# Kernel optimization log

Hardware: AMD Instinct MI355X
Metric: run time of the kernel (lower is better)

The kernel has to match this reference:

```python
import jax, jax.numpy as jnp
import numpy as np

N_HEAD = 16
ROPE_BASE = 10000.0


def _rotate_every_two(x):
    # x: [..., d]; pairs (x0,x1) -> (-x1, x0) interleaved (GPT-J style)
    x1 = x[..., ::2]
    x2 = x[..., 1::2]
    return jnp.stack((-x2, x1), axis=-1).reshape(x.shape)


def _rope_cos_sin(T, head_dim, dtype):
    inv_freq = 1.0 / (ROPE_BASE ** (jnp.arange(0, head_dim, 2, dtype=jnp.float32) / head_dim))
    t = jnp.arange(T, dtype=jnp.float32)
    freqs = t[:, None] * inv_freq[None, :]            # [T, hd/2]
    emb = jnp.repeat(freqs, 2, axis=-1)               # [T, hd], each freq duplicated
    return jnp.cos(emb).astype(dtype)[None, None], jnp.sin(emb).astype(dtype)[None, None]


def setup_inputs() -> dict:
    key = jax.random.key(0)
    k1, k2, k3 = jax.random.split(key, 3)
    C = 2048
    x = jax.random.normal(k1, (2, 2048, C), dtype=jnp.float32)
    Wqkv = jax.random.normal(k2, (C, 3 * C), dtype=jnp.float32) * 0.02   # c_attn.weight^T
    Wproj = jax.random.normal(k3, (C, C), dtype=jnp.float32) * 0.02      # c_proj.weight^T
    return {"x": x, "Wqkv": Wqkv, "Wproj": Wproj, "causal": 1}


def reference(x, Wqkv, Wproj, causal):
    B, T, C = x.shape
    H = N_HEAD
    hd = C // H

    qkv = x @ Wqkv                                    # [B,T,3C]
    q, k, v = jnp.split(qkv, 3, axis=-1)
    # -> [B,H,T,hd]
    q = q.reshape(B, T, H, hd).transpose(0, 2, 1, 3)
    k = k.reshape(B, T, H, hd).transpose(0, 2, 1, 3)
    v = v.reshape(B, T, H, hd).transpose(0, 2, 1, 3)

    cos, sin = _rope_cos_sin(T, hd, x.dtype)          # [1,1,T,hd]
    q = q * cos + _rotate_every_two(q) * sin
    k = k * cos + _rotate_every_two(k) * sin

    scale = 1.0 / jnp.sqrt(jnp.asarray(hd, dtype=x.dtype))
    scores = jnp.einsum('bhqd,bhkd->bhqk', q, k) * scale  # [B,H,T,T]
    if causal:
        mask = jnp.tril(jnp.ones((T, T), dtype=bool))
        scores = jnp.where(mask[None, None], scores, jnp.asarray(-1e30, dtype=scores.dtype))
    attn = jax.nn.softmax(scores, axis=-1)
    y = jnp.einsum('bhqk,bhkd->bhqd', attn, v)        # [B,H,T,hd]
    y = y.transpose(0, 2, 1, 3).reshape(B, T, C)
    return y @ Wproj
```

## Files before the change

### kernel.cpp

```cpp
#include <hip/hip_runtime.h>
#include <cmath>

typedef __bf16 bf16_t;
typedef __bf16 bf16x8 __attribute__((ext_vector_type(8)));
typedef __bf16 bf16x4 __attribute__((ext_vector_type(4)));
typedef float f32x4 __attribute__((ext_vector_type(4)));

#define T_SEQ 2048
#define C_DIM 2048
#define H_NUM 16
#define HD    128
#define KK    2048

__global__ void rope_table_kernel(float* __restrict__ ct, float* __restrict__ st) {
  int idx = blockIdx.x * 256 + threadIdx.x;
  int t = idx >> 6, i = idx & 63;
  double invf = pow(10000.0, -(double)i / 64.0);
  float ang = (float)t * (float)invf;
  ct[idx] = cosf(ang);
  st[idx] = sinf(ang);
}

__global__ void convert_bf16_kernel(const float* __restrict__ in, bf16_t* __restrict__ out, int n4) {
  int i = blockIdx.x * 256 + threadIdx.x;
  if (i >= n4) return;
  const float4 v = reinterpret_cast<const float4*>(in)[i];
  bf16x4 o;
  o[0] = (bf16_t)v.x; o[1] = (bf16_t)v.y; o[2] = (bf16_t)v.z; o[3] = (bf16_t)v.w;
  reinterpret_cast<bf16x4*>(out)[i] = o;
}

__global__ void transpose_convert_kernel(const float* __restrict__ in, bf16_t* __restrict__ out,
                                         int R, int Cc) {
  __shared__ __align__(16) bf16_t tile[32][33];
  int c0 = blockIdx.x * 32, r0 = blockIdx.y * 32;
  int tx = threadIdx.x, ty = threadIdx.y;
#pragma unroll
  for (int i = 0; i < 4; ++i)
    tile[ty + 8 * i][tx] = (bf16_t)in[(size_t)(r0 + ty + 8 * i) * Cc + c0 + tx];
  __syncthreads();
#pragma unroll
  for (int i = 0; i < 4; ++i)
    out[(size_t)(c0 + ty + 8 * i) * R + r0 + tx] = tile[tx][ty + 8 * i];
}

template <int MODE>
__global__ __launch_bounds__(256, 2)
void gemm_bf16_kernel(const bf16_t* __restrict__ A, const bf16_t* __restrict__ Bt,
                      float* __restrict__ outF,
                      bf16_t* __restrict__ qws, bf16_t* __restrict__ kws,
                      bf16_t* __restrict__ vtws,
                      const float* __restrict__ ctab, const float* __restrict__ stab) {
  const int tid = threadIdx.x;
  const int l = tid & 63, w = tid >> 6;
  const int wr = w >> 1, wc = w & 1;
  const int lg = l >> 4, lr = l & 15;

  const int g = blockIdx.x & 7;
  const int q = blockIdx.x >> 3;
  int m0, n0;
  if (MODE == 0) {
    m0 = (q / 6) * 128;
    n0 = (g * 6 + (q % 6)) * 128;
  } else {
    m0 = (g * 4 + (q & 3)) * 128;
    n0 = (q >> 2) * 128;
  }

  __shared__ __align__(16) bf16_t la[128][64];
  __shared__ __align__(16) bf16_t lb[128][64];

  f32x4 acc[4][4] = {};
  bf16x8 ra[4], rb[4];

  const bf16_t* Ab = A + (size_t)m0 * KK;
  const bf16_t* Bb = Bt + (size_t)n0 * KK;

#pragma unroll
  for (int c = 0; c < 4; ++c) {
    int p = tid + c * 256, row = p >> 3, kc = p & 7;
    ra[c] = *reinterpret_cast<const bf16x8*>(Ab + (size_t)row * KK + kc * 8);
    rb[c] = *reinterpret_cast<const bf16x8*>(Bb + (size_t)row * KK + kc * 8);
  }

  for (int kt = 0; kt < KK / 64; ++kt) {
    __syncthreads();
#pragma unroll
    for (int c = 0; c < 4; ++c) {
      int p = tid + c * 256, row = p >> 3;
      int kcw = (p & 7) ^ (row & 7);
      *reinterpret_cast<bf16x8*>(&la[row][kcw * 8]) = ra[c];
      *reinterpret_cast<bf16x8*>(&lb[row][kcw * 8]) = rb[c];
    }
    __syncthreads();
    if (kt + 1 < KK / 64) {
#pragma unroll
      for (int c = 0; c < 4; ++c) {
        int p = tid + c * 256, row = p >> 3, kc = p & 7;
        ra[c] = *reinterpret_cast<const bf16x8*>(Ab + (size_t)row * KK + (kt + 1) * 64 + kc * 8);
        rb[c] = *reinterpret_cast<const bf16x8*>(Bb + (size_t)row * KK + (kt + 1) * 64 + kc * 8);
      }
    }
#pragma unroll
    for (int ks = 0; ks < 2; ++ks) {
      bf16x8 af[4], bfr[4];
      const int pc = ((ks * 4 + lg) ^ (lr & 7)) * 8;
#pragma unroll
      for (int i = 0; i < 4; ++i) {
        af[i]  = *reinterpret_cast<const bf16x8*>(&la[wr * 64 + i * 16 + lr][pc]);
        bfr[i] = *reinterpret_cast<const bf16x8*>(&lb[wc * 64 + i * 16 + lr][pc]);
      }
#pragma unroll
      for (int mi = 0; mi < 4; ++mi)
#pragma unroll
        for (int ni = 0; ni < 4; ++ni)
          acc[mi][ni] = __builtin_amdgcn_mfma_f32_16x16x32_bf16(af[mi], bfr[ni], acc[mi][ni], 0, 0, 0);
    }
  }

  if (MODE == 0) {
    const int sec = n0 >> 11;
    const int h = (n0 & 2047) >> 7;
#pragma unroll
    for (int mi = 0; mi < 4; ++mi) {
#pragma unroll
      for (int ni = 0; ni < 4; ++ni) {
        const int d = wc * 64 + ni * 16 + lr;
#pragma unroll
        for (int r = 0; r < 4; ++r) {
          const int m = m0 + wr * 64 + mi * 16 + lg * 4 + r;
          const int b = m >> 11, t = m & 2047;
          float val = acc[mi][ni][r];
          if (sec < 2) {
            float partner = __shfl_xor(val, 1);
            const int fi = d >> 1;
            float cth = ctab[t * 64 + fi], sth = stab[t * 64 + fi];
            float ov = (d & 1) ? (val * cth + partner * sth)
                               : (val * cth - partner * sth);
            if (sec == 0) ov *= 0.127517445f;
            bf16_t* dst = (sec == 0) ? qws : kws;
            dst[((size_t)(b * H_NUM + h) * T_SEQ + t) * HD + d] = (bf16_t)ov;
          } else {
            vtws[((size_t)(b * H_NUM + h) * HD + d) * T_SEQ + t] = (bf16_t)val;
          }
        }
      }
    }
  } else {
#pragma unroll
    for (int mi = 0; mi < 4; ++mi)
#pragma unroll
      for (int ni = 0; ni < 4; ++ni) {
        const int n = n0 + wc * 64 + ni * 16 + lr;
#pragma unroll
        for (int r = 0; r < 4; ++r) {
          const int m = m0 + wr * 64 + mi * 16 + lg * 4 + r;
          outF[(size_t)m * C_DIM + n] = acc[mi][ni][r];
        }
      }
  }
}

__global__ __launch_bounds__(256, 2)
void attention_kernel(const bf16_t* __restrict__ qg, const bf16_t* __restrict__ kg,
                      const bf16_t* __restrict__ vtg, bf16_t* __restrict__ yg) {
  const int tid = threadIdx.x;
  const int l = tid & 63, w = tid >> 6;
  const int lg = l >> 4, lr = l & 15;

  const int g = blockIdx.x & 7;
  const int j = blockIdx.x >> 3;
  const int bh = 4 * g + (j >> 4);
  const int pair = j & 15;
  const int b = bh >> 4, h = bh & 15;

  __shared__ __align__(16) bf16_t lk[2][64][128];
  __shared__ __align__(16) bf16_t lp[4][16][72];

  const bf16_t* qp = qg + (size_t)bh * T_SEQ * HD;
  const bf16_t* kp = kg + (size_t)bh * T_SEQ * HD;
  const bf16_t* vp = vtg + (size_t)bh * HD * T_SEQ;

#pragma unroll 1
  for (int half = 0; half < 2; ++half) {
    const int qt = (half == 0) ? (31 - pair) : pair;
    const int qbase = qt * 64 + w * 16;

    bf16x8 qf[4];
#pragma unroll
    for (int dk = 0; dk < 4; ++dk)
      qf[dk] = *reinterpret_cast<const bf16x8*>(qp + (size_t)(qbase + lr) * HD + dk * 32 + lg * 8);

    f32x4 o[8] = {};
    float mrun = -1e30f, lrun = 0.f;

    bf16x8 kreg[4];
#pragma unroll
    for (int c = 0; c < 4; ++c) {
      int p = tid + c * 256, row = p >> 4, ch = p & 15;
      kreg[c] = *reinterpret_cast<const bf16x8*>(kp + (size_t)row * HD + ch * 8);
    }
    __syncthreads();
#pragma unroll
    for (int c = 0; c < 4; ++c) {
      int p = tid + c * 256, row = p >> 4, ch = (p & 15) ^ (row & 7);
      *reinterpret_cast<bf16x8*>(&lk[0][row][ch * 8]) = kreg[c];
    }
    __syncthreads();

#pragma unroll 1
    for (int kt = 0; kt <= qt; ++kt) {
      const int cur = kt & 1;
      const int kv0 = kt * 64;

      bf16x8 vf[16];
#pragma unroll
      for (int cc = 0; cc < 8; ++cc)
#pragma unroll
        for (int ks = 0; ks < 2; ++ks)
          vf[cc * 2 + ks] = *reinterpret_cast<const bf16x8*>(
              vp + (size_t)(cc * 16 + lr) * T_SEQ + kv0 + ks * 32 + lg * 8);

      if (kt < qt) {
#pragma unroll
        for (int c = 0; c < 4; ++c) {
          int p = tid + c * 256, row = p >> 4, ch = p & 15;
          kreg[c] = *reinterpret_cast<const bf16x8*>(
              kp + (size_t)(kv0 + 64 + row) * HD + ch * 8);
        }
      }

      f32x4 sacc[4] = {};
#pragma unroll
      for (int dk = 0; dk < 4; ++dk) {
        bf16x8 kf[4];
#pragma unroll
        for (int f = 0; f < 4; ++f) {
          const int ch = (dk * 4 + lg) ^ (lr & 7);
          kf[f] = *reinterpret_cast<const bf16x8*>(&lk[cur][f * 16 + lr][ch * 8]);
        }
        __builtin_amdgcn_s_setprio(1);
#pragma unroll
        for (int f = 0; f < 4; ++f)
          sacc[f] = __builtin_amdgcn_mfma_f32_16x16x32_bf16(kf[f], qf[dk], sacc[f], 0, 0, 0);
        __builtin_amdgcn_s_setprio(0);
      }

      if (kt == qt) {
#pragma unroll
        for (int f = 0; f < 4; ++f)
#pragma unroll
          for (int r = 0; r < 4; ++r)
            if (kv0 + f * 16 + lg * 4 + r > qbase + lr) sacc[f][r] = -1e30f;
      }

      float mloc = sacc[0][0];
#pragma unroll
      for (int f = 0; f < 4; ++f)
#pragma unroll
        for (int r = 0; r < 4; ++r) mloc = fmaxf(mloc, sacc[f][r]);
      mloc = fmaxf(mloc, __shfl_xor(mloc, 16));
      mloc = fmaxf(mloc, __shfl_xor(mloc, 32));

      if (__any(mloc > mrun + 8.f)) {
        float mnew = fmaxf(mrun, mloc);
        float sf = exp2f(mrun - mnew);
        mrun = mnew;
        lrun *= sf;
        float sfr[4];
#pragma unroll
        for (int r = 0; r < 4; ++r)
          sfr[r] = __shfl(sf, (l & 48) | (lg * 4 + r));
#pragma unroll
        for (int cc = 0; cc < 8; ++cc)
#pragma unroll
          for (int r = 0; r < 4; ++r) o[cc][r] *= sfr[r];
      }

      float ssum = 0.f;
#pragma unroll
      for (int f = 0; f < 4; ++f)
#pragma unroll
        for (int r = 0; r < 4; ++r) {
          sacc[f][r] = exp2f(sacc[f][r] - mrun);
          ssum += sacc[f][r];
        }
      ssum += __shfl_xor(ssum, 16);
      ssum += __shfl_xor(ssum, 32);
      lrun += ssum;

#pragma unroll
      for (int f = 0; f < 4; ++f) {
        bf16x4 pk;
#pragma unroll
        for (int r = 0; r < 4; ++r) pk[r] = (bf16_t)sacc[f][r];
        *reinterpret_cast<bf16x4*>(&lp[w][lr][f * 16 + lg * 4]) = pk;
      }

#pragma unroll
      for (int ks = 0; ks < 2; ++ks) {
        bf16x8 pf = *reinterpret_cast<const bf16x8*>(&lp[w][lr][ks * 32 + lg * 8]);
        __builtin_amdgcn_s_setprio(1);
#pragma unroll
        for (int cc = 0; cc < 8; ++cc)
          o[cc] = __builtin_amdgcn_mfma_f32_16x16x32_bf16(pf, vf[cc * 2 + ks], o[cc], 0, 0, 0);
        __builtin_amdgcn_s_setprio(0);
      }

      if (kt < qt) {
#pragma unroll
        for (int c = 0; c < 4; ++c) {
          int p = tid + c * 256, row = p >> 4, ch = (p & 15) ^ (row & 7);
          *reinterpret_cast<bf16x8*>(&lk[cur ^ 1][row][ch * 8]) = kreg[c];
        }
      }
      __syncthreads();
    }

    float linv = 1.0f / lrun;
    float linvr[4];
#pragma unroll
    for (int r = 0; r < 4; ++r)
      linvr[r] = __shfl(linv, (l & 48) | (lg * 4 + r));
#pragma unroll
    for (int cc = 0; cc < 8; ++cc)
#pragma unroll
      for (int r = 0; r < 4; ++r) {
        int t = qbase + lg * 4 + r;
        float val = o[cc][r] * linvr[r];
        yg[((size_t)(b * T_SEQ + t)) * C_DIM + h * HD + cc * 16 + lr] = (bf16_t)val;
      }
  }
}

extern "C" void kernel_launch(void* const* d_in, const int* in_sizes, int n_in,
                              void* d_out, int out_size, void* d_ws, size_t ws_size,
                              hipStream_t stream) {
  (void)in_sizes; (void)n_in; (void)out_size; (void)ws_size;
  const float* x     = (const float*)d_in[0];
  const float* Wqkv  = (const float*)d_in[1];
  const float* Wproj = (const float*)d_in[2];
  float* out = (float*)d_out;

  char* ws = (char*)d_ws;
  float*  ctab   = (float*)(ws + 0);
  float*  stab   = (float*)(ws + 524288);
  bf16_t* xb     = (bf16_t*)(ws + 1048576);
  bf16_t* wqkvT  = (bf16_t*)(ws + 17825792);
  bf16_t* wprojT = (bf16_t*)(ws + 42991616);
  bf16_t* qws    = (bf16_t*)(ws + 51380224);
  bf16_t* kws    = (bf16_t*)(ws + 68157440);
  bf16_t* vtws   = (bf16_t*)(ws + 84934656);
  bf16_t* yws    = (bf16_t*)(ws + 101711872);

  rope_table_kernel<<<512, 256, 0, stream>>>(ctab, stab);
  convert_bf16_kernel<<<8192, 256, 0, stream>>>(x, xb, 2097152);
  transpose_convert_kernel<<<dim3(192, 64), dim3(32, 8), 0, stream>>>(Wqkv, wqkvT, 2048, 6144);
  transpose_convert_kernel<<<dim3(64, 64), dim3(32, 8), 0, stream>>>(Wproj, wprojT, 2048, 2048);

  gemm_bf16_kernel<0><<<1536, 256, 0, stream>>>(
      xb, wqkvT, nullptr, qws, kws, vtws, ctab, stab);

  attention_kernel<<<512, 256, 0, stream>>>(qws, kws, vtws, yws);

  gemm_bf16_kernel<1><<<512, 256, 0, stream>>>(
      yws, wprojT, out, nullptr, nullptr, nullptr, nullptr, nullptr);
}
```

Baseline: 357.0 us.

## Load K directly from global into registers and split attention into one q-tile per block

Measured after the change: 551.0 us. 1.54x slower.

```diff
diff --git a/kernel.cpp b/kernel.cpp
--- a/kernel.cpp
+++ b/kernel.cpp
@@ -161,7 +161,7 @@
   }
 }
 
-__global__ __launch_bounds__(256, 2)
+__global__ __launch_bounds__(256, 3)
 void attention_kernel(const bf16_t* __restrict__ qg, const bf16_t* __restrict__ kg,
                       const bf16_t* __restrict__ vtg, bf16_t* __restrict__ yg) {
   const int tid = threadIdx.x;
@@ -170,167 +170,146 @@
 
   const int g = blockIdx.x & 7;
   const int j = blockIdx.x >> 3;
-  const int bh = 4 * g + (j >> 4);
-  const int pair = j & 15;
+  const int bh = 4 * g + (j >> 5);
+  const int qt = 31 - (j & 31);
   const int b = bh >> 4, h = bh & 15;
-
-  __shared__ __align__(16) bf16_t lk[2][64][128];
+  const int qbase = qt * 64 + w * 16;
+
   __shared__ __align__(16) bf16_t lp[4][16][72];
 
   const bf16_t* qp = qg + (size_t)bh * T_SEQ * HD;
   const bf16_t* kp = kg + (size_t)bh * T_SEQ * HD;
   const bf16_t* vp = vtg + (size_t)bh * HD * T_SEQ;
 
+  bf16x8 qf[4];
+#pragma unroll
+  for (int dk = 0; dk < 4; ++dk)
+    qf[dk] = *reinterpret_cast<const bf16x8*>(qp + (size_t)(qbase + lr) * HD + dk * 32 + lg * 8);
+
+  f32x4 o[8] = {};
+  float mrun = -1e30f, lrun = 0.f;
+
 #pragma unroll 1
-  for (int half = 0; half < 2; ++half) {
-    const int qt = (half == 0) ? (31 - pair) : pair;
-    const int qbase = qt * 64 + w * 16;
-
-    bf16x8 qf[4];
-#pragma unroll
-    for (int dk = 0; dk < 4; ++dk)
-      qf[dk] = *reinterpret_cast<const bf16x8*>(qp + (size_t)(qbase + lr) * HD + dk * 32 + lg * 8);
-
-    f32x4 o[8] = {};
-    float mrun = -1e30f, lrun = 0.f;
-
-    bf16x8 kreg[4];
-#pragma unroll
-    for (int c = 0; c < 4; ++c) {
-      int p = tid + c * 256, row = p >> 4, ch = p & 15;
-      kreg[c] = *reinterpret_cast<const bf16x8*>(kp + (size_t)row * HD + ch * 8);
-    }
-    __syncthreads();
-#pragma unroll
-    for (int c = 0; c < 4; ++c) {
-      int p = tid + c * 256, row = p >> 4, ch = (p & 15) ^ (row & 7);
-      *reinterpret_cast<bf16x8*>(&lk[0][row][ch * 8]) = kreg[c];
-    }
-    __syncthreads();
-
-#pragma unroll 1
-    for (int kt = 0; kt <= qt; ++kt) {
-      const int cur = kt & 1;
-      const int kv0 = kt * 64;
-
-      bf16x8 vf[16];
+  for (int kt = 0; kt <= qt; ++kt) {
+    const int kv0 = kt * 64;
+
+    bf16x8 vf0[8];
+#pragma unroll
+    for (int cc = 0; cc < 8; ++cc)
+      vf0[cc] = *reinterpret_cast<const bf16x8*>(
+          vp + (size_t)(cc * 16 + lr) * T_SEQ + kv0 + lg * 8);
+
+    f32x4 sacc[4] = {};
+    bf16x8 kfa[4], kfb[4];
+#pragma unroll
+    for (int f = 0; f < 4; ++f)
+      kfa[f] = *reinterpret_cast<const bf16x8*>(
+          kp + (size_t)(kv0 + f * 16 + lr) * HD + lg * 8);
+#pragma unroll
+    for (int dk = 0; dk < 4; ++dk) {
+      if (dk < 3) {
+#pragma unroll
+        for (int f = 0; f < 4; ++f)
+          kfb[f] = *reinterpret_cast<const bf16x8*>(
+              kp + (size_t)(kv0 + f * 16 + lr) * HD + (dk + 1) * 32 + lg * 8);
+      }
+      __builtin_amdgcn_s_setprio(1);
+#pragma unroll
+      for (int f = 0; f < 4; ++f)
+        sacc[f] = __builtin_amdgcn_mfma_f32_16x16x32_bf16(kfa[f], qf[dk], sacc[f], 0, 0, 0);
+      __builtin_amdgcn_s_setprio(0);
+#pragma unroll
+      for (int f = 0; f < 4; ++f) kfa[f] = kfb[f];
+    }
+
+    bf16x8 vf1[8];
+#pragma unroll
+    for (int cc = 0; cc < 8; ++cc)
+      vf1[cc] = *reinterpret_cast<const bf16x8*>(
+          vp + (size_t)(cc * 16 + lr) * T_SEQ + kv0 + 32 + lg * 8);
+
+    if (kt == qt) {
+#pragma unroll
+      for (int f = 0; f < 4; ++f)
+#pragma unroll
+        for (int r = 0; r < 4; ++r)
+          if (kv0 + f * 16 + lg * 4 + r > qbase + lr) sacc[f][r] = -1e30f;
+    }
+
+    float mloc = sacc[0][0];
+#pragma unroll
+    for (int f = 0; f < 4; ++f)
+#pragma unroll
+      for (int r = 0; r < 4; ++r) mloc = fmaxf(mloc, sacc[f][r]);
+    mloc = fmaxf(mloc, __shfl_xor(mloc, 16));
+    mloc = fmaxf(mloc, __shfl_xor(mloc, 32));
+
+    if (__any(mloc > mrun + 8.f)) {
+      float mnew = fmaxf(mrun, mloc);
+      float sf = exp2f(mrun - mnew);
+      mrun = mnew;
+      lrun *= sf;
+      float sfr[4];
+#pragma unroll
+      for (int r = 0; r < 4; ++r)
+        sfr[r] = __shfl(sf, (l & 48) | (lg * 4 + r));
 #pragma unroll
       for (int cc = 0; cc < 8; ++cc)
 #pragma unroll
-        for (int ks = 0; ks < 2; ++ks)
-          vf[cc * 2 + ks] = *reinterpret_cast<const bf16x8*>(
-              vp + (size_t)(cc * 16 + lr) * T_SEQ + kv0 + ks * 32 + lg * 8);
-
-      if (kt < qt) {
-#pragma unroll
-        for (int c = 0; c < 4; ++c) {
-          int p = tid + c * 256, row = p >> 4, ch = p & 15;
-          kreg[c] = *reinterpret_cast<const bf16x8*>(
-              kp + (size_t)(kv0 + 64 + row) * HD + ch * 8);
-        }
-      }
-
-      f32x4 sacc[4] = {};
-#pragma unroll
-      for (int dk = 0; dk < 4; ++dk) {
-        bf16x8 kf[4];
-#pragma unroll
-        for (int f = 0; f < 4; ++f) {
-          const int ch = (dk * 4 + lg) ^ (lr & 7);
-          kf[f] = *reinterpret_cast<const bf16x8*>(&lk[cur][f * 16 + lr][ch * 8]);
-        }
-        __builtin_amdgcn_s_setprio(1);
-#pragma unroll
-        for (int f = 0; f < 4; ++f)
-          sacc[f] = __builtin_amdgcn_mfma_f32_16x16x32_bf16(kf[f], qf[dk], sacc[f], 0, 0, 0);
-        __builtin_amdgcn_s_setprio(0);
-      }
-
-      if (kt == qt) {
-#pragma unroll
-        for (int f = 0; f < 4; ++f)
-#pragma unroll
-          for (int r = 0; r < 4; ++r)
-            if (kv0 + f * 16 + lg * 4 + r > qbase + lr) sacc[f][r] = -1e30f;
-      }
-
-      float mloc = sacc[0][0];
-#pragma unroll
-      for (int f = 0; f < 4; ++f)
-#pragma unroll
-        for (int r = 0; r < 4; ++r) mloc = fmaxf(mloc, sacc[f][r]);
-      mloc = fmaxf(mloc, __shfl_xor(mloc, 16));
-      mloc = fmaxf(mloc, __shfl_xor(mloc, 32));
-
-      if (__any(mloc > mrun + 8.f)) {
-        float mnew = fmaxf(mrun, mloc);
-        float sf = exp2f(mrun - mnew);
-        mrun = mnew;
-        lrun *= sf;
-        float sfr[4];
-#pragma unroll
-        for (int r = 0; r < 4; ++r)
-          sfr[r] = __shfl(sf, (l & 48) | (lg * 4 + r));
-#pragma unroll
-        for (int cc = 0; cc < 8; ++cc)
-#pragma unroll
-          for (int r = 0; r < 4; ++r) o[cc][r] *= sfr[r];
-      }
-
-      float ssum = 0.f;
-#pragma unroll
-      for (int f = 0; f < 4; ++f)
-#pragma unroll
-        for (int r = 0; r < 4; ++r) {
-          sacc[f][r] = exp2f(sacc[f][r] - mrun);
-          ssum += sacc[f][r];
-        }
-      ssum += __shfl_xor(ssum, 16);
-      ssum += __shfl_xor(ssum, 32);
-      lrun += ssum;
-
-#pragma unroll
-      for (int f = 0; f < 4; ++f) {
-        bf16x4 pk;
-#pragma unroll
-        for (int r = 0; r < 4; ++r) pk[r] = (bf16_t)sacc[f][r];
-        *reinterpret_cast<bf16x4*>(&lp[w][lr][f * 16 + lg * 4]) = pk;
-      }
-
-#pragma unroll
-      for (int ks = 0; ks < 2; ++ks) {
-        bf16x8 pf = *reinterpret_cast<const bf16x8*>(&lp[w][lr][ks * 32 + lg * 8]);
-        __builtin_amdgcn_s_setprio(1);
-#pragma unroll
-        for (int cc = 0; cc < 8; ++cc)
-          o[cc] = __builtin_amdgcn_mfma_f32_16x16x32_bf16(pf, vf[cc * 2 + ks], o[cc], 0, 0, 0);
-        __builtin_amdgcn_s_setprio(0);
-      }
-
-      if (kt < qt) {
-#pragma unroll
-        for (int c = 0; c < 4; ++c) {
-          int p = tid + c * 256, row = p >> 4, ch = (p & 15) ^ (row & 7);
-          *reinterpret_cast<bf16x8*>(&lk[cur ^ 1][row][ch * 8]) = kreg[c];
-        }
-      }
-      __syncthreads();
-    }
-
-    float linv = 1.0f / lrun;
-    float linvr[4];
-#pragma unroll
-    for (int r = 0; r < 4; ++r)
-      linvr[r] = __shfl(linv, (l & 48) | (lg * 4 + r));
-#pragma unroll
-    for (int cc = 0; cc < 8; ++cc)
+        for (int r = 0; r < 4; ++r) o[cc][r] *= sfr[r];
+    }
+
+    float ssum = 0.f;
+#pragma unroll
+    for (int f = 0; f < 4; ++f)
 #pragma unroll
       for (int r = 0; r < 4; ++r) {
-        int t = qbase + lg * 4 + r;
-        float val = o[cc][r] * linvr[r];
-        yg[((size_t)(b * T_SEQ + t)) * C_DIM + h * HD + cc * 16 + lr] = (bf16_t)val;
-      }
-  }
+        sacc[f][r] = exp2f(sacc[f][r] - mrun);
+        ssum += sacc[f][r];
+      }
+    ssum += __shfl_xor(ssum, 16);
+    ssum += __shfl_xor(ssum, 32);
+    lrun += ssum;
+
+#pragma unroll
+    for (int f = 0; f < 4; ++f) {
+      bf16x4 pk;
+#pragma unroll
+      for (int r = 0; r < 4; ++r) pk[r] = (bf16_t)sacc[f][r];
+      *reinterpret_cast<bf16x4*>(&lp[w][lr][f * 16 + lg * 4]) = pk;
+    }
+
+    {
+      bf16x8 pf = *reinterpret_cast<const bf16x8*>(&lp[w][lr][lg * 8]);
+      __builtin_amdgcn_s_setprio(1);
+#pragma unroll
+      for (int cc = 0; cc < 8; ++cc)
+        o[cc] = __builtin_amdgcn_mfma_f32_16x16x32_bf16(pf, vf0[cc], o[cc], 0, 0, 0);
+      __builtin_amdgcn_s_setprio(0);
+    }
+    {
+      bf16x8 pf = *reinterpret_cast<const bf16x8*>(&lp[w][lr][32 + lg * 8]);
+      __builtin_amdgcn_s_setprio(1);
+#pragma unroll
+      for (int cc = 0; cc < 8; ++cc)
+        o[cc] = __builtin_amdgcn_mfma_f32_16x16x32_bf16(pf, vf1[cc], o[cc], 0, 0, 0);
+      __builtin_amdgcn_s_setprio(0);
+    }
+  }
+
+  float linv = 1.0f / lrun;
+  float linvr[4];
+#pragma unroll
+  for (int r = 0; r < 4; ++r)
+    linvr[r] = __shfl(linv, (l & 48) | (lg * 4 + r));
+#pragma unroll
+  for (int cc = 0; cc < 8; ++cc)
+#pragma unroll
+    for (int r = 0; r < 4; ++r) {
+      int t = qbase + lg * 4 + r;
+      float val = o[cc][r] * linvr[r];
+      yg[((size_t)(b * T_SEQ + t)) * C_DIM + h * HD + cc * 16 + lr] = (bf16_t)val;
+    }
 }
 
 extern "C" void kernel_launch(void* const* d_in, const int* in_sizes, int n_in,
@@ -361,7 +340,7 @@
   gemm_bf16_kernel<0><<<1536, 256, 0, stream>>>(
       xb, wqkvT, nullptr, qws, kws, vtws, ctab, stab);
 
-  attention_kernel<<<512, 256, 0, stream>>>(qws, kws, vtws, yws);
+  attention_kernel<<<1024, 256, 0, stream>>>(qws, kws, vtws, yws);
 
   gemm_bf16_kernel<1><<<512, 256, 0, stream>>>(
       yws, wprojT, out, nullptr, nullptr, nullptr, nullptr, nullptr);
```

## Process 128-key tiles per iteration with single-buffered LDS for K

Applied to the files above, without the earlier changes.

Result: slower. 433.0 us (+21.3%).

```diff
diff --git a/kernel.cpp b/kernel.cpp
--- a/kernel.cpp
+++ b/kernel.cpp
@@ -174,8 +174,8 @@
   const int pair = j & 15;
   const int b = bh >> 4, h = bh & 15;
 
-  __shared__ __align__(16) bf16_t lk[2][64][128];
-  __shared__ __align__(16) bf16_t lp[4][16][72];
+  __shared__ __align__(16) bf16_t lk[128][128];
+  __shared__ __align__(16) bf16_t lp[4][16][136];
 
   const bf16_t* qp = qg + (size_t)bh * T_SEQ * HD;
   const bf16_t* kp = kg + (size_t)bh * T_SEQ * HD;
@@ -185,6 +185,7 @@
   for (int half = 0; half < 2; ++half) {
     const int qt = (half == 0) ? (31 - pair) : pair;
     const int qbase = qt * 64 + w * 16;
+    const int nit = (qt + 2) >> 1;
 
     bf16x8 qf[4];
 #pragma unroll
@@ -194,61 +195,77 @@
     f32x4 o[8] = {};
     float mrun = -1e30f, lrun = 0.f;
 
-    bf16x8 kreg[4];
-#pragma unroll
-    for (int c = 0; c < 4; ++c) {
+    bf16x8 kreg[8];
+#pragma unroll
+    for (int c = 0; c < 8; ++c) {
       int p = tid + c * 256, row = p >> 4, ch = p & 15;
       kreg[c] = *reinterpret_cast<const bf16x8*>(kp + (size_t)row * HD + ch * 8);
     }
     __syncthreads();
 #pragma unroll
-    for (int c = 0; c < 4; ++c) {
+    for (int c = 0; c < 8; ++c) {
       int p = tid + c * 256, row = p >> 4, ch = (p & 15) ^ (row & 7);
-      *reinterpret_cast<bf16x8*>(&lk[0][row][ch * 8]) = kreg[c];
+      *reinterpret_cast<bf16x8*>(&lk[row][ch * 8]) = kreg[c];
     }
     __syncthreads();
 
 #pragma unroll 1
-    for (int kt = 0; kt <= qt; ++kt) {
-      const int cur = kt & 1;
-      const int kv0 = kt * 64;
-
-      bf16x8 vf[16];
+    for (int kt = 0; kt < nit; ++kt) {
+      const int kv0 = kt * 128;
+
+      bf16x8 vfA[16];
 #pragma unroll
       for (int cc = 0; cc < 8; ++cc)
 #pragma unroll
         for (int ks = 0; ks < 2; ++ks)
-          vf[cc * 2 + ks] = *reinterpret_cast<const bf16x8*>(
+          vfA[cc * 2 + ks] = *reinterpret_cast<const bf16x8*>(
               vp + (size_t)(cc * 16 + lr) * T_SEQ + kv0 + ks * 32 + lg * 8);
 
-      if (kt < qt) {
-#pragma unroll
-        for (int c = 0; c < 4; ++c) {
+      if (kt + 1 < nit) {
+#pragma unroll
+        for (int c = 0; c < 8; ++c) {
           int p = tid + c * 256, row = p >> 4, ch = p & 15;
           kreg[c] = *reinterpret_cast<const bf16x8*>(
-              kp + (size_t)(kv0 + 64 + row) * HD + ch * 8);
-        }
-      }
-
-      f32x4 sacc[4] = {};
+              kp + (size_t)(kv0 + 128 + row) * HD + ch * 8);
+        }
+      }
+
+      f32x4 sacc[8] = {};
 #pragma unroll
       for (int dk = 0; dk < 4; ++dk) {
-        bf16x8 kf[4];
-#pragma unroll
-        for (int f = 0; f < 4; ++f) {
+        bf16x8 kf[8];
+#pragma unroll
+        for (int f = 0; f < 8; ++f) {
           const int ch = (dk * 4 + lg) ^ (lr & 7);
-          kf[f] = *reinterpret_cast<const bf16x8*>(&lk[cur][f * 16 + lr][ch * 8]);
+          kf[f] = *reinterpret_cast<const bf16x8*>(&lk[f * 16 + lr][ch * 8]);
         }
         __builtin_amdgcn_s_setprio(1);
 #pragma unroll
-        for (int f = 0; f < 4; ++f)
+        for (int f = 0; f < 8; ++f)
           sacc[f] = __builtin_amdgcn_mfma_f32_16x16x32_bf16(kf[f], qf[dk], sacc[f], 0, 0, 0);
         __builtin_amdgcn_s_setprio(0);
       }
-
-      if (kt == qt) {
-#pragma unroll
-        for (int f = 0; f < 4; ++f)
+      __syncthreads();
+
+      if (kt + 1 < nit) {
+#pragma unroll
+        for (int c = 0; c < 8; ++c) {
+          int p = tid + c * 256, row = p >> 4, ch = (p & 15) ^ (row & 7);
+          *reinterpret_cast<bf16x8*>(&lk[row][ch * 8]) = kreg[c];
+        }
+      }
+
+      bf16x8 vfB[16];
+#pragma unroll
+      for (int cc = 0; cc < 8; ++cc)
+#pragma unroll
+        for (int ks = 0; ks < 2; ++ks)
+          vfB[cc * 2 + ks] = *reinterpret_cast<const bf16x8*>(
+              vp + (size_t)(cc * 16 + lr) * T_SEQ + kv0 + 64 + ks * 32 + lg * 8);
+
+      if (kt == nit - 1) {
+#pragma unroll
+        for (int f = 0; f < 8; ++f)
 #pragma unroll
           for (int r = 0; r < 4; ++r)
             if (kv0 + f * 16 + lg * 4 + r > qbase + lr) sacc[f][r] = -1e30f;
@@ -256,7 +273,7 @@
 
       float mloc = sacc[0][0];
 #pragma unroll
-      for (int f = 0; f < 4; ++f)
+      for (int f = 0; f < 8; ++f)
 #pragma unroll
         for (int r = 0; r < 4; ++r) mloc = fmaxf(mloc, sacc[f][r]);
       mloc = fmaxf(mloc, __shfl_xor(mloc, 16));
@@ -279,7 +296,7 @@
 
       float ssum = 0.f;
 #pragma unroll
-      for (int f = 0; f < 4; ++f)
+      for (int f = 0; f < 8; ++f)
 #pragma unroll
         for (int r = 0; r < 4; ++r) {
           sacc[f][r] = exp2f(sacc[f][r] - mrun);
@@ -290,7 +307,7 @@
       lrun += ssum;
 
 #pragma unroll
-      for (int f = 0; f < 4; ++f) {
+      for (int f = 0; f < 8; ++f) {
         bf16x4 pk;
 #pragma unroll
         for (int r = 0; r < 4; ++r) pk[r] = (bf16_t)sacc[f][r];
@@ -303,17 +320,19 @@
         __builtin_amdgcn_s_setprio(1);
 #pragma unroll
         for (int cc = 0; cc < 8; ++cc)
-          o[cc] = __builtin_amdgcn_mfma_f32_16x16x32_bf16(pf, vf[cc * 2 + ks], o[cc], 0, 0, 0);
+          o[cc] = __builtin_amdgcn_mfma_f32_16x16x32_bf16(pf, vfA[cc * 2 + ks], o[cc], 0, 0, 0);
         __builtin_amdgcn_s_setprio(0);
       }
-
-      if (kt < qt) {
-#pragma unroll
-        for (int c = 0; c < 4; ++c) {
-          int p = tid + c * 256, row = p >> 4, ch = (p & 15) ^ (row & 7);
-          *reinterpret_cast<bf16x8*>(&lk[cur ^ 1][row][ch * 8]) = kreg[c];
-        }
-      }
+#pragma unroll
+      for (int ks = 2; ks < 4; ++ks) {
+        bf16x8 pf = *reinterpret_cast<const bf16x8*>(&lp[w][lr][ks * 32 + lg * 8]);
+        __builtin_amdgcn_s_setprio(1);
+#pragma unroll
+        for (int cc = 0; cc < 8; ++cc)
+          o[cc] = __builtin_amdgcn_mfma_f32_16x16x32_bf16(pf, vfB[cc * 2 + (ks - 2)], o[cc], 0, 0, 0);
+        __builtin_amdgcn_s_setprio(0);
+      }
+
       __syncthreads();
     }
 
```
